# Kernel tuning notes

Measured on AMD Instinct MI355X. Metric: run time of the kernel, lower is better.

Reference implementation:

```python
import jax, jax.numpy as jnp
import numpy as np

# ---- static config (matches init_kwargs) ----
B = 8            # batch_size (graphs)
N = 10000        # num_nodes per graph
NTOT = B * N     # total node rows (80000)
E = 320000       # edges (only over first N nodes, as in the original code)
D = 128          # input_dim == backbone_channels (shared conv forces equality)
H = 4            # heads
C = 128          # backbone_channels (per-head out dim, concat=False)
L = 3            # num_backbone_layers
K = 30           # sort-pool k
HID = 512        # mlp_hidden_dim
OUT = 2          # output_dim
EXPECTED = K * L * C * H + 1  # buggy mlp_input_dim from __init__ -> zero-pad
BN_EPS = 1e-5


def setup_inputs() -> dict:
    key = jax.random.key(0)
    ks = jax.random.split(key, 20)
    s = 1.0 / np.sqrt(D)
    inp = {
        "x": jax.random.normal(ks[0], (NTOT, D), dtype=jnp.float32),
        "edge_index": jax.random.randint(ks[1], (2, E), 0, N, dtype=jnp.int32),
        "age": jax.random.normal(ks[2], (B,), dtype=jnp.float32),
        # shared TransformerConv params (reused across all L layers)
        "Wq": jax.random.normal(ks[3], (D, H * C), dtype=jnp.float32) * s,
        "bq": jax.random.normal(ks[4], (H * C,), dtype=jnp.float32) * 0.02,
        "Wk": jax.random.normal(ks[5], (D, H * C), dtype=jnp.float32) * s,
        "bk": jax.random.normal(ks[6], (H * C,), dtype=jnp.float32) * 0.02,
        "Wv": jax.random.normal(ks[7], (D, H * C), dtype=jnp.float32) * s,
        "bv": jax.random.normal(ks[8], (H * C,), dtype=jnp.float32) * 0.02,
        "Wskip": jax.random.normal(ks[9], (D, C), dtype=jnp.float32) * s,
        "bskip": jax.random.normal(ks[10], (C,), dtype=jnp.float32) * 0.02,
        # per-layer BatchNorm (eval mode: running stats)
        "bn_gamma": 1.0 + 0.1 * jax.random.normal(ks[11], (L, C), dtype=jnp.float32),
        "bn_beta": 0.1 * jax.random.normal(ks[12], (L, C), dtype=jnp.float32),
        "bn_mean": 0.1 * jax.random.normal(ks[13], (L, C), dtype=jnp.float32),
        "bn_var": jax.random.uniform(ks[14], (L, C), dtype=jnp.float32, minval=0.5, maxval=1.5),
        # MLP head (2 layers: EXPECTED->HID, ReLU, HID->OUT)
        "W1": jax.random.normal(ks[15], (EXPECTED, HID), dtype=jnp.float32) * (1.0 / np.sqrt(EXPECTED)),
        "b1": jnp.zeros((HID,), dtype=jnp.float32),
        "W2": jax.random.normal(ks[16], (HID, OUT), dtype=jnp.float32) * (1.0 / np.sqrt(HID)),
        "b2": jnp.zeros((OUT,), dtype=jnp.float32),
    }
    return inp


def _transformer_conv(h, src, dst, Wq, bq, Wk, bk, Wv, bv, Wskip, bskip):
    # PyG TransformerConv, concat=False, root_weight=True, eval (no attn dropout)
    q = (h @ Wq + bq).reshape(NTOT, H, C)
    k = (h @ Wk + bk).reshape(NTOT, H, C)
    v = (h @ Wv + bv).reshape(NTOT, H, C)
    # per-edge attention logits [E, H]
    alpha = jnp.einsum("ehc,ehc->eh", q[dst], k[src]) / np.sqrt(C).astype(np.float32)
    # segment softmax over incoming edges of each target node
    m = jax.ops.segment_max(alpha, dst, num_segments=NTOT)          # [NTOT, H]
    e = jnp.exp(alpha - m[dst])
    denom = jax.ops.segment_sum(e, dst, num_segments=NTOT)          # [NTOT, H]
    a = e / (denom[dst] + 1e-16)                                    # [E, H]
    out = jax.ops.segment_sum(a[:, :, None] * v[src], dst, num_segments=NTOT)  # [NTOT,H,C]
    return out.mean(axis=1) + h @ Wskip + bskip                     # concat=False -> head mean


def reference(x, edge_index, age, Wq, bq, Wk, bk, Wv, bv, Wskip, bskip,
              bn_gamma, bn_beta, bn_mean, bn_var, W1, b1, W2, b2):
    src, dst = edge_index[0], edge_index[1]
    h = x
    feats = []
    for i in range(L):  # fixed small layer count; shared conv weights
        h = _transformer_conv(h, src, dst, Wq, bq, Wk, bk, Wv, bv, Wskip, bskip)
        h = (h - bn_mean[i]) * (bn_gamma[i] / jnp.sqrt(bn_var[i] + BN_EPS)) + bn_beta[i]
        h = jax.nn.relu(h)  # dropout: eval mode no-op
        feats.append(h)
    h = feats[-1]  # concat_input_graph=False
    # global_sort_pool: sort nodes per graph by last channel (desc), take top-k
    xr = h.reshape(B, N, C)
    idx = jnp.argsort(-xr[:, :, -1], axis=1)[:, :K]                 # [B, K]
    pooled = jnp.take_along_axis(xr, idx[:, :, None], axis=1)       # [B, K, C]
    z = pooled.reshape(B, K * C)
    z = jnp.concatenate([z, age.reshape(B, 1)], axis=1)             # [B, K*C+1]
    # zero-pad to the (mismatched) expected MLP input dim, as in the original
    z = jnp.concatenate([z, jnp.zeros((B, EXPECTED - z.shape[1]), dtype=z.dtype)], axis=1)
    z = jax.nn.relu(z @ W1 + b1)
    z = z @ W2 + b2
    return jax.nn.log_softmax(z, axis=-1)
```

## Files before the change

kernel.cpp:

```cpp
#include <hip/hip_runtime.h>
#include <cmath>


#define NN    10000
#define NTOT  80000
#define EE    320000
#define CH    128

__device__ __forceinline__ float rl_f(float v, int lane) {
    return __uint_as_float(__builtin_amdgcn_readlane(__float_as_uint(v), lane));
}

__global__ __launch_bounds__(256) void precompute_kernel(
    const float* __restrict__ Wq, const float* __restrict__ bq,
    const float* __restrict__ Wk, const float* __restrict__ Wv,
    const float* __restrict__ bv, const float* __restrict__ Wskip,
    const float* __restrict__ bskip,
    const float* __restrict__ bn_gamma, const float* __restrict__ bn_beta,
    const float* __restrict__ bn_mean, const float* __restrict__ bn_var,
    float* __restrict__ Bcat, float* __restrict__ biascat,
    float* __restrict__ Wcomb, float* __restrict__ bvbar,
    float* __restrict__ bnS, float* __restrict__ bnB)
{
    const float inv_sqrtC = 0.08838834764831845f;
    int idx = blockIdx.x * 256 + threadIdx.x;
    if (idx < 65536) {
        int c = idx >> 9;
        int o = idx & 511;
        int hbase = o & ~127;
        int j = o & 127;
        const float* wq = Wq + c * 512 + hbase;
        const float* wk = Wk + j * 512 + hbase;
        float s = 0.f;
        for (int cc = 0; cc < 128; cc++) s = fmaf(wq[cc], wk[cc], s);
        Bcat[c * 640 + o] = s * inv_sqrtC;
        return;
    }
    idx -= 65536;
    if (idx < 16384) {
        int c = idx >> 7, n = idx & 127;
        Bcat[c * 640 + 512 + n] = Wskip[c * 128 + n];
        return;
    }
    idx -= 16384;
    if (idx < 512) {
        int o = idx, hbase = o & ~127, j = o & 127;
        const float* wk = Wk + j * 512 + hbase;
        const float* bqp = bq + hbase;
        float s = 0.f;
        for (int cc = 0; cc < 128; cc++) s = fmaf(bqp[cc], wk[cc], s);
        biascat[o] = s * inv_sqrtC;
        return;
    }
    idx -= 512;
    if (idx < 128) {
        biascat[512 + idx] = bskip[idx];
        return;
    }
    idx -= 128;
    if (idx < 65536) {
        int k = idx >> 7;
        int n = idx & 127;
        int h = k >> 7, c = k & 127;
        Wcomb[k * 128 + n] = Wv[c * 512 + h * 128 + n] * 0.25f;
        return;
    }
    idx -= 65536;
    if (idx < 128) {
        float s = 0.f;
        for (int h = 0; h < 4; h++) s += bv[h * 128 + idx];
        bvbar[idx] = 0.25f * s;
        return;
    }
    idx -= 128;
    if (idx < 384) {
        float sc = bn_gamma[idx] / sqrtf(bn_var[idx] + 1e-5f);
        bnS[idx] = sc;
        bnB[idx] = bn_beta[idx] - bn_mean[idx] * sc;
        return;
    }
}

__global__ void count_kernel(const int* __restrict__ dst, int* __restrict__ deg) {
    int e = blockIdx.x * 256 + threadIdx.x;
    if (e < EE) atomicAdd(&deg[dst[e]], 1);
}

__global__ __launch_bounds__(1024) void scan_kernel(const int* __restrict__ deg,
                                                    int* __restrict__ rowstart) {
    __shared__ int part[1024];
    const int t = threadIdx.x;
    int loc[10];
    int s = 0;
    for (int i = 0; i < 10; i++) {
        int idx = t * 10 + i;
        int v = (idx < NN) ? deg[idx] : 0;
        loc[i] = s; s += v;
    }
    part[t] = s; __syncthreads();
    for (int d = 1; d < 1024; d <<= 1) {
        int v = (t >= d) ? part[t - d] : 0;
        __syncthreads();
        part[t] += v;
        __syncthreads();
    }
    int base = (t == 0) ? 0 : part[t - 1];
    for (int i = 0; i < 10; i++) {
        int idx = t * 10 + i;
        if (idx <= NN) rowstart[idx] = base + loc[i];
    }
}

__global__ void scatter_kernel(const int* __restrict__ src, const int* __restrict__ dst,
                               const int* __restrict__ rowstart, int* __restrict__ cursor,
                               int* __restrict__ csr_src) {
    int e = blockIdx.x * 256 + threadIdx.x;
    if (e < EE) {
        int d = dst[e];
        int p = atomicAdd(&cursor[d], 1);
        csr_src[rowstart[d] + p] = src[e];
    }
}

__global__ __launch_bounds__(256, 3) void skip_keys_kernel(
    const float* __restrict__ xup,
    const float* __restrict__ Wskip,
    const float* __restrict__ bskip,
    const float* __restrict__ bnS, const float* __restrict__ bnB,
    float* __restrict__ gkeys)
{
    __shared__ float rowb[64][132];
    __shared__ float Bs[16][132];
    __shared__ float sWc[128];
    const int t = threadIdx.x;
    const int r0 = blockIdx.x * 64;
    const int Mrem = min(64, (NTOT - NN) - r0);
    const int tx = t & 15;
    const int ty = t >> 4;

    for (int f = t; f < 64 * 32; f += 256) {
        int row = f >> 5, c4 = (f & 31) * 4;
        if (row < Mrem)
            *(float4*)&rowb[row][c4] = *(const float4*)(xup + (size_t)(r0 + row) * CH + c4);
    }
    if (t < 128) sWc[t] = Wskip[t * 128 + 127];

    for (int l = 0; l < 2; l++) {
        float acc[4][8];
        #pragma unroll
        for (int i = 0; i < 4; i++)
            #pragma unroll
            for (int j = 0; j < 8; j++) acc[i][j] = 0.f;

        for (int k0 = 0; k0 < 128; k0 += 16) {
            __syncthreads();
            for (int f = t; f < 512; f += 256) {
                int kk = f >> 5, n4 = (f & 31) * 4;
                *(float4*)&Bs[kk][n4] = *(const float4*)(Wskip + (size_t)(k0 + kk) * 128 + n4);
            }
            __syncthreads();
            #pragma unroll
            for (int kq = 0; kq < 4; kq++) {
                float4 a4[4];
                #pragma unroll
                for (int i = 0; i < 4; i++)
                    a4[i] = *(const float4*)&rowb[ty + 16 * i][k0 + kq * 4];
                float4 c0[4], c1[4];
                #pragma unroll
                for (int q = 0; q < 4; q++) {
                    c0[q] = *(const float4*)&Bs[kq * 4 + q][tx * 4];
                    c1[q] = *(const float4*)&Bs[kq * 4 + q][64 + tx * 4];
                }
                #pragma unroll
                for (int q = 0; q < 4; q++) {
                    #pragma unroll
                    for (int i = 0; i < 4; i++) {
                        const float av = (q == 0) ? a4[i].x : (q == 1) ? a4[i].y
                                       : (q == 2) ? a4[i].z : a4[i].w;
                        acc[i][0] = fmaf(av, c0[q].x, acc[i][0]);
                        acc[i][1] = fmaf(av, c0[q].y, acc[i][1]);
                        acc[i][2] = fmaf(av, c0[q].z, acc[i][2]);
                        acc[i][3] = fmaf(av, c0[q].w, acc[i][3]);
                        acc[i][4] = fmaf(av, c1[q].x, acc[i][4]);
                        acc[i][5] = fmaf(av, c1[q].y, acc[i][5]);
                        acc[i][6] = fmaf(av, c1[q].z, acc[i][6]);
                        acc[i][7] = fmaf(av, c1[q].w, acc[i][7]);
                    }
                }
            }
        }
        __syncthreads();
        const float* bS = bnS + l * 128;
        const float* bB = bnB + l * 128;
        #pragma unroll
        for (int i = 0; i < 4; i++) {
            const int row = ty + 16 * i;
            float4 v0, v1;
            float* p0 = &v0.x;
            float* p1 = &v1.x;
            #pragma unroll
            for (int q = 0; q < 4; q++) {
                const int n0c = tx * 4 + q;
                float xv = acc[i][q] + bskip[n0c];
                xv = fmaf(xv, bS[n0c], bB[n0c]);
                p0[q] = fmaxf(xv, 0.f);
                const int n1c = 64 + tx * 4 + q;
                float yv = acc[i][4 + q] + bskip[n1c];
                yv = fmaf(yv, bS[n1c], bB[n1c]);
                p1[q] = fmaxf(yv, 0.f);
            }
            *(float4*)&rowb[row][tx * 4] = v0;
            *(float4*)&rowb[row][64 + tx * 4] = v1;
        }
    }
    __syncthreads();
    if (t < Mrem) {
        float s = 0.f;
        for (int k = 0; k < 128; k++) s = fmaf(rowb[t][k], sWc[k], s);
        s += bskip[127];
        s = fmaf(s, bnS[2 * 128 + 127], bnB[2 * 128 + 127]);
        gkeys[NN + r0 + t] = fmaxf(s, 0.f);
    }
}

template<int BM, int BN, int TM, int TN, int MODE>
__global__ __launch_bounds__(256) void gemm_fp32(
    const float* __restrict__ A, int lda,
    const float* __restrict__ B, int ldb,
    const float* __restrict__ bias, const float* __restrict__ bias2,
    const int* __restrict__ deg,
    const float* __restrict__ Cold,
    const float* __restrict__ bnS, const float* __restrict__ bnB,
    float* __restrict__ C0, int ldc0,
    float* __restrict__ C1, int ldc1,
    int M, int K,
    float* __restrict__ keysOut)
{
    constexpr int BK = 16;
    __shared__ float As[BK][BM + 4];
    __shared__ float Bs[BK][BN + 4];
    const int t  = threadIdx.x;
    const int tx = t % (BN / TN);
    const int ty = t / (BN / TN);
    const int m0 = blockIdx.x * BM;
    const int n0 = blockIdx.y * BN;
    float acc[TM][TN];
    #pragma unroll
    for (int i = 0; i < TM; i++)
        #pragma unroll
        for (int j = 0; j < TN; j++) acc[i][j] = 0.f;

    for (int k0 = 0; k0 < K; k0 += BK) {
        #pragma unroll
        for (int f = t; f < BM * 4; f += 256) {
            int row = f >> 2, fc = f & 3;
            int gm = m0 + row;
            float4 v = make_float4(0.f, 0.f, 0.f, 0.f);
            if (gm < M) v = *(const float4*)(A + (size_t)gm * lda + k0 + fc * 4);
            As[fc * 4 + 0][row] = v.x;
            As[fc * 4 + 1][row] = v.y;
            As[fc * 4 + 2][row] = v.z;
            As[fc * 4 + 3][row] = v.w;
        }
        #pragma unroll
        for (int f = t; f < BK * (BN / 4); f += 256) {
            int kk = f / (BN / 4);
            int nn = (f % (BN / 4)) * 4;
            *(float4*)(&Bs[kk][nn]) = *(const float4*)(B + (size_t)(k0 + kk) * ldb + n0 + nn);
        }
        __syncthreads();
        #pragma unroll
        for (int kk = 0; kk < BK; kk++) {
            float af[TM], bf[TN];
            if constexpr (TM == 2) {
                float2 v = *(const float2*)&As[kk][ty * 2];
                af[0] = v.x; af[1] = v.y;
            } else {
                float4 v = *(const float4*)&As[kk][ty * 4];
                af[0] = v.x; af[1] = v.y; af[2] = v.z; af[3] = v.w;
            }
            if constexpr (TN == 4) {
                float4 v = *(const float4*)&Bs[kk][tx * 4];
                bf[0] = v.x; bf[1] = v.y; bf[2] = v.z; bf[3] = v.w;
            } else {
                float4 v = *(const float4*)&Bs[kk][tx * 4];
                float4 w = *(const float4*)&Bs[kk][BN / 2 + tx * 4];
                bf[0] = v.x; bf[1] = v.y; bf[2] = v.z; bf[3] = v.w;
                bf[4] = w.x; bf[5] = w.y; bf[6] = w.z; bf[7] = w.w;
            }
            #pragma unroll
            for (int i = 0; i < TM; i++)
                #pragma unroll
                for (int j = 0; j < TN; j++)
                    acc[i][j] = fmaf(af[i], bf[j], acc[i][j]);
        }
        __syncthreads();
    }
    #pragma unroll
    for (int i = 0; i < TM; i++) {
        const int gm = m0 + ty * TM + i;
        if (gm >= M) continue;
        const bool addB2 = (MODE == 4) ? (deg[gm] > 0) : false;
        #pragma unroll
        for (int h = 0; h < TN / 4; h++) {
            const int nb = n0 + ((TN == 8) ? h * (BN / 2) + tx * 4 : tx * TN + h * 4);
            float4 v;
            float* vp = &v.x;
            if (MODE == 4) {
                const float4 old = *(const float4*)(Cold + (size_t)gm * ldc1 + nb);
                const float* op = &old.x;
                #pragma unroll
                for (int q = 0; q < 4; q++) {
                    const int n = nb + q;
                    float x = acc[i][h * 4 + q] + op[q];
                    if (addB2) x += bias2[n];
                    x = fmaf(x, bnS[n], bnB[n]);
                    vp[q] = fmaxf(x, 0.f);
                }
                *(float4*)(C0 + (size_t)gm * ldc0 + nb) = v;
                if (keysOut != nullptr && nb == 124) keysOut[gm] = v.w;
            } else {
                #pragma unroll
                for (int q = 0; q < 4; q++)
                    vp[q] = acc[i][h * 4 + q] + bias[nb + q];
                if (nb < 512)
                    *(float4*)(C0 + (size_t)gm * ldc0 + nb) = v;
                else
                    *(float4*)(C1 + (size_t)gm * ldc1 + nb - 512) = v;
            }
        }
    }
}

__global__ __launch_bounds__(256) void attn_kernel(
    const float* __restrict__ h,
    const float* __restrict__ u,
    float* __restrict__ g,
    const int* __restrict__ rowstart,
    const int* __restrict__ csr_src)
{
    __shared__ float h_lds[128 * 65];
    __shared__ __align__(16) float palpha[4 * 64 * 4];
    __shared__ __align__(16) float wT[64 * 4];
    __shared__ __align__(16) float scale_lds[4];
    __shared__ __align__(16) float s_lds[4];
    __shared__ __align__(16) float merge[128 * 4];
    __shared__ int src_lds[64];

    const int n  = blockIdx.x;
    const int t  = threadIdx.x;
    const int w  = t >> 6;
    const int l  = t & 63;
    const int c  = t & 127;
    const int jh = t >> 7;
    const int rs   = rowstart[n];
    const int degn = rowstart[n + 1] - rs;

    if (degn == 0) {
        g[(size_t)n * 512 + t] = 0.f;
        g[(size_t)n * 512 + 256 + t] = 0.f;
        return;
    }
    float u_reg0 = u[(size_t)n * 512 + ((l >> 5)) * 128 + 32 * w + (l & 31)];
    float u_reg1 = u[(size_t)n * 512 + ((l >> 5) + 2) * 128 + 32 * w + (l & 31)];

    float m_run = -INFINITY, s_run = 0.f;
    float4 acc4 = make_float4(0.f, 0.f, 0.f, 0.f);

    for (int base = 0; base < degn; base += 64) {
        const int len = min(64, degn - base);
        __syncthreads();
        if (t < len) src_lds[t] = csr_src[rs + base + t];
        __syncthreads();
        for (int f = t; f < len * 128; f += 256) {
            const int cc = f & 127, j = f >> 7;
            h_lds[cc * 65 + j] = h[(size_t)src_lds[j] * CH + cc];
        }
        __syncthreads();
        {
            float p0 = 0.f, p1 = 0.f, p2 = 0.f, p3 = 0.f;
            #pragma unroll
            for (int dc = 0; dc < 32; dc++) {
                const float hv = h_lds[(32 * w + dc) * 65 + l];
                p0 = fmaf(rl_f(u_reg0, dc),      hv, p0);
                p1 = fmaf(rl_f(u_reg0, 32 + dc), hv, p1);
                p2 = fmaf(rl_f(u_reg1, dc),      hv, p2);
                p3 = fmaf(rl_f(u_reg1, 32 + dc), hv, p3);
            }
            palpha[(0 * 64 + l) * 4 + w] = p0;
            palpha[(1 * 64 + l) * 4 + w] = p1;
            palpha[(2 * 64 + l) * 4 + w] = p2;
            palpha[(3 * 64 + l) * 4 + w] = p3;
        }
        __syncthreads();
        {
            const float4 pa = *(const float4*)&palpha[(w * 64 + l) * 4];
            float alpha = (l < len) ? (pa.x + pa.y + pa.z + pa.w) : -INFINITY;
            float mx = alpha;
            #pragma unroll
            for (int d = 1; d < 64; d <<= 1) mx = fmaxf(mx, __shfl_xor(mx, d, 64));
            const float newm = fmaxf(m_run, mx);
            float e = (l < len) ? __expf(alpha - newm) : 0.f;
            float ss = e;
            #pragma unroll
            for (int d = 1; d < 64; d <<= 1) ss += __shfl_xor(ss, d, 64);
            const float sc = (m_run == -INFINITY) ? 0.f : __expf(m_run - newm);
            s_run = s_run * sc + ss;
            m_run = newm;
            wT[l * 4 + w] = e;
            if (l == 0) scale_lds[w] = sc;
        }
        __syncthreads();
        {
            const float4 scv = *(const float4*)scale_lds;
            acc4.x *= scv.x; acc4.y *= scv.y; acc4.z *= scv.z; acc4.w *= scv.w;
            const int j0 = jh * 32;
            const int j1 = min(len, j0 + 32);
            for (int j = j0; j < j1; j++) {
                const float hv = h_lds[c * 65 + j];
                const float4 wv = *(const float4*)&wT[j * 4];
                acc4.x = fmaf(wv.x, hv, acc4.x);
                acc4.y = fmaf(wv.y, hv, acc4.y);
                acc4.z = fmaf(wv.z, hv, acc4.z);
                acc4.w = fmaf(wv.w, hv, acc4.w);
            }
        }
    }
    if (l == 0) s_lds[w] = s_run;
    __syncthreads();
    if (jh == 1) *(float4*)&merge[c * 4] = acc4;
    __syncthreads();
    if (jh == 0) {
        const float4 o  = *(const float4*)&merge[c * 4];
        const float4 sv = *(const float4*)s_lds;
        g[(size_t)n * 512 + 0 * 128 + c] = (acc4.x + o.x) / (sv.x + 1e-16f);
        g[(size_t)n * 512 + 1 * 128 + c] = (acc4.y + o.y) / (sv.y + 1e-16f);
        g[(size_t)n * 512 + 2 * 128 + c] = (acc4.z + o.z) / (sv.z + 1e-16f);
        g[(size_t)n * 512 + 3 * 128 + c] = (acc4.w + o.w) / (sv.w + 1e-16f);
    }
}

__global__ __launch_bounds__(256) void radix_pool_kernel(
    const float* __restrict__ gkeys, const float* __restrict__ age,
    int* __restrict__ sel, float* __restrict__ z)
{
    __shared__ unsigned int keys[NN];
    __shared__ int hist[256];
    __shared__ int sbuf[256];
    __shared__ unsigned int sel_prefix;
    __shared__ int sel_need;
    __shared__ int gt_counter;
    __shared__ unsigned int cand_key[30];
    __shared__ int cand_idx[30];
    __shared__ int order[30];

    const int b = blockIdx.x;
    const int t = threadIdx.x;

    for (int i = t; i < NN; i += 256)
        keys[i] = __float_as_uint(gkeys[(size_t)b * NN + i]);
    if (t == 0) { sel_prefix = 0u; sel_need = 30; gt_counter = 0; }
    __syncthreads();

    for (int r = 3; r >= 0; r--) {
        hist[t] = 0;
        __syncthreads();
        const int shift = r * 8;
        const unsigned int pmask = (r == 3) ? 0u : (0xFFFFFFFFu << ((r + 1) * 8));
        const unsigned int pref = sel_prefix;
        const int need = sel_need;
        for (int i = t; i < NN; i += 256) {
            unsigned int k = keys[i];
            if ((k & pmask) == pref)
                atomicAdd(&hist[(k >> shift) & 255u], 1);
        }
        __syncthreads();
        sbuf[t] = hist[255 - t];
        __syncthreads();
        for (int d = 1; d < 256; d <<= 1) {
            int o = (t >= d) ? sbuf[t - d] : 0;
            __syncthreads();
            sbuf[t] += o;
            __syncthreads();
        }
        {
            const int v = t;
            const int ge = sbuf[255 - v];
            const int gt = ge - hist[v];
            if (gt < need && need <= ge) {
                sel_prefix = pref | ((unsigned int)v << shift);
                sel_need = need - gt;
            }
        }
        __syncthreads();
    }

    const unsigned int T = sel_prefix;
    const int need_eq = sel_need;
    const int n_gt = 30 - need_eq;

    for (int i = t; i < NN; i += 256) {
        unsigned int k = keys[i];
        if (k > T) {
            int p = atomicAdd(&gt_counter, 1);
            cand_key[p] = k; cand_idx[p] = i;
        }
    }
    {
        const int CHK = (NN + 255) / 256;
        const int i0 = t * CHK, i1 = min(NN, i0 + CHK);
        int local = 0;
        for (int i = i0; i < i1; i++) if (keys[i] == T) local++;
        sbuf[t] = local;
        __syncthreads();
        for (int d = 1; d < 256; d <<= 1) {
            int o = (t >= d) ? sbuf[t - d] : 0;
            __syncthreads();
            sbuf[t] += o;
            __syncthreads();
        }
        int rank = (t == 0) ? 0 : sbuf[t - 1];
        for (int i = i0; i < i1; i++) {
            if (keys[i] == T) {
                if (rank < need_eq) { cand_key[n_gt + rank] = T; cand_idx[n_gt + rank] = i; }
                rank++;
            }
        }
    }
    __syncthreads();
    if (t < 30) {
        const unsigned int mk = cand_key[t];
        const int mi = cand_idx[t];
        int rk = 0;
        for (int j = 0; j < 30; j++) {
            const unsigned int ok = cand_key[j];
            const int oi = cand_idx[j];
            if (ok > mk || (ok == mk && oi < mi)) rk++;
        }
        order[rk] = t;
    }
    __syncthreads();
    if (t < 30) sel[b * 30 + t] = cand_idx[order[t]];
    if (t == 0) z[(size_t)b * 3841 + 3840] = age[b];
}

__global__ __launch_bounds__(128) void gather_kernel(
    const float* __restrict__ h3,
    const float* __restrict__ x,
    const float* __restrict__ Wskip, const float* __restrict__ bskip,
    const float* __restrict__ bnS, const float* __restrict__ bnB,
    const int* __restrict__ sel, float* __restrict__ z)
{
    __shared__ float buf0[128], buf1[128];
    const int blk = blockIdx.x;
    const int b = blk / 30;
    const int kk = blk % 30;
    const int c = threadIdx.x;
    const int i = sel[b * 30 + kk];
    const size_t g = (size_t)b * NN + i;
    float v;
    if (b == 0) {
        v = h3[g * CH + c];
    } else {
        float* rd = buf0;
        float* wr = buf1;
        buf0[c] = x[g * CH + c];
        __syncthreads();
        float s = 0.f;
        for (int l = 0; l < 3; l++) {
            s = 0.f;
            for (int k = 0; k < 128; k++) s = fmaf(rd[k], Wskip[k * 128 + c], s);
            s += bskip[c];
            s = fmaf(s, bnS[l * 128 + c], bnB[l * 128 + c]);
            s = fmaxf(s, 0.f);
            if (l < 2) {
                wr[c] = s;
                __syncthreads();
                float* tmp = rd; rd = wr; wr = tmp;
            }
        }
        v = s;
    }
    z[(size_t)b * 3841 + kk * CH + c] = v;
}

__global__ __launch_bounds__(256) void mlp1_kernel(
    const float* __restrict__ z, const float* __restrict__ W1,
    float* __restrict__ zh)
{
    __shared__ float zs[256];
    const int b  = blockIdx.x >> 4;
    const int ic = blockIdx.x & 15;
    const int t  = threadIdx.x;
    const int i0 = ic * 241;
    const int i1 = min(3841, i0 + 241);
    float a0 = 0.f, a1 = 0.f;
    for (int cb = i0; cb < i1; cb += 256) {
        int cl = min(256, i1 - cb);
        __syncthreads();
        if (t < cl) zs[t] = z[(size_t)b * 3841 + cb + t];
        __syncthreads();
        #pragma unroll 4
        for (int q = 0; q < cl; q++) {
            float zv = zs[q];
            const float* wp = W1 + (size_t)(cb + q) * 512;
            a0 = fmaf(zv, wp[t], a0);
            a1 = fmaf(zv, wp[t + 256], a1);
        }
    }
    atomicAdd(&zh[(size_t)b * 512 + t], a0);
    atomicAdd(&zh[(size_t)b * 512 + t + 256], a1);
}

__global__ __launch_bounds__(256) void mlp2_kernel(
    const float* __restrict__ zh, const float* __restrict__ b1,
    const float* __restrict__ W2, const float* __restrict__ b2,
    float* __restrict__ out)
{
    __shared__ float r0[256], r1[256];
    const int b = blockIdx.x;
    const int t = threadIdx.x;
    float a0 = 0.f, a1 = 0.f;
    for (int j = t; j < 512; j += 256) {
        float v = fmaxf(zh[(size_t)b * 512 + j] + b1[j], 0.f);
        a0 = fmaf(v, W2[j * 2 + 0], a0);
        a1 = fmaf(v, W2[j * 2 + 1], a1);
    }
    r0[t] = a0; r1[t] = a1; __syncthreads();
    for (int s = 128; s > 0; s >>= 1) {
        if (t < s) { r0[t] += r0[t + s]; r1[t] += r1[t + s]; }
        __syncthreads();
    }
    if (t == 0) {
        float l0 = r0[0] + b2[0], l1 = r1[0] + b2[1];
        float m = fmaxf(l0, l1);
        float lse = m + logf(__expf(l0 - m) + __expf(l1 - m));
        out[b * 2 + 0] = l0 - lse;
        out[b * 2 + 1] = l1 - lse;
    }
}

extern "C" void kernel_launch(void* const* d_in, const int* in_sizes, int n_in,
                              void* d_out, int out_size, void* d_ws, size_t ws_size,
                              hipStream_t stream) {
    const float* x     = (const float*)d_in[0];
    const int*   ei    = (const int*)d_in[1];
    const float* age   = (const float*)d_in[2];
    const float* Wq    = (const float*)d_in[3];
    const float* bq    = (const float*)d_in[4];
    const float* Wk    = (const float*)d_in[5];
    const float* Wv    = (const float*)d_in[7];
    const float* bv    = (const float*)d_in[8];
    const float* Wskip = (const float*)d_in[9];
    const float* bskip = (const float*)d_in[10];
    const float* bn_g  = (const float*)d_in[11];
    const float* bn_b  = (const float*)d_in[12];
    const float* bn_m  = (const float*)d_in[13];
    const float* bn_v  = (const float*)d_in[14];
    const float* W1    = (const float*)d_in[15];
    const float* b1    = (const float*)d_in[16];
    const float* W2    = (const float*)d_in[17];
    const float* b2    = (const float*)d_in[18];

    float* ws = (float*)d_ws;
    float* h3      = ws;
    float* hlowA   = h3 + 10240000;
    float* hlowB   = hlowA + 1280000;
    float* u       = hlowB + 1280000;
    float* skipraw = u + 5120000;
    float* Bcat    = skipraw + 1280000;
    float* biascat = Bcat + 81920;
    float* Wcomb   = biascat + 640;
    float* bvbar   = Wcomb + 65536;
    float* bnS     = bvbar + 128;
    float* bnB     = bnS + 384;
    float* zbuf    = bnB + 384;
    float* zh      = zbuf + 30728;
    int* deg      = (int*)(zh + 4096);
    int* cursor   = deg + NN;
    int* rowstart = cursor + NN;
    int* csr_src  = rowstart + NN + 1;
    float* keysG  = (float*)(csr_src + EE);
    int* sel      = (int*)(keysG + NTOT);

    const int* srcI = ei;
    const int* dstI = ei + EE;

    hipMemsetAsync(deg, 0, sizeof(int) * (2 * NN), stream);
    hipMemsetAsync(zh, 0, sizeof(float) * 4096, stream);

    precompute_kernel<<<581, 256, 0, stream>>>(Wq, bq, Wk, Wv, bv, Wskip, bskip,
                                               bn_g, bn_b, bn_m, bn_v,
                                               Bcat, biascat, Wcomb, bvbar, bnS, bnB);
    count_kernel<<<1250, 256, 0, stream>>>(dstI, deg);
    scan_kernel<<<1, 1024, 0, stream>>>(deg, rowstart);
    scatter_kernel<<<1250, 256, 0, stream>>>(srcI, dstI, rowstart, cursor, csr_src);

    skip_keys_kernel<<<1094, 256, 0, stream>>>(x + (size_t)NN * CH, Wskip, bskip,
                                               bnS, bnB, keysG);

    const float* hcur = x;
    for (int l = 0; l < 3; l++) {
        float* dest = (l == 0) ? hlowA : (l == 1) ? hlowB : h3;
        gemm_fp32<64, 128, 4, 8, 0><<<dim3(157, 5), 256, 0, stream>>>(
            hcur, CH, Bcat, 640, biascat, nullptr, nullptr, nullptr,
            nullptr, nullptr, u, 512, skipraw, CH, NN, 128, nullptr);
        attn_kernel<<<NN, 256, 0, stream>>>(hcur, u, u, rowstart, csr_src);
        gemm_fp32<32, 64, 2, 4, 4><<<dim3(313, 2), 256, 0, stream>>>(
            u, 512, Wcomb, CH, nullptr, bvbar, deg, skipraw,
            bnS + l * 128, bnB + l * 128, dest, CH, nullptr, CH, NN, 512,
            (l == 2) ? keysG : nullptr);
        hcur = dest;
    }
    radix_pool_kernel<<<8, 256, 0, stream>>>(keysG, age, sel, zbuf);
    gather_kernel<<<240, 128, 0, stream>>>(h3, x, Wskip, bskip,
                                           bnS, bnB, sel, zbuf);
    mlp1_kernel<<<128, 256, 0, stream>>>(zbuf, W1, zh);
    mlp2_kernel<<<8, 256, 0, stream>>>(zh, b1, W2, b2, (float*)d_out);
}
```

Measured before the change: 624.6 us.

## Replace tiled fp32 GEMMs with row-per-lane kernels reading weights as wave-uniform scalars

The skip-keys GEMM and the two per-layer GEMMs are rewritten so each lane owns one row and each wave owns a 32- or 8-column slice. Weight reads become wave-uniform addresses the compiler can serve through scalar loads, which removes the shared-memory staging of B tiles and most barriers. Results are staged in LDS so stores stay coalesced. The trade-off is lower arithmetic intensity per thread and repeated global or scalar-cache reads of the weights in every block, and the combine kernel is re-gridded to 157x4 blocks.

```diff
diff --git a/kernel.cpp b/kernel.cpp
--- a/kernel.cpp
+++ b/kernel.cpp
@@ -122,7 +122,7 @@
     }
 }
 
-__global__ __launch_bounds__(256, 3) void skip_keys_kernel(
+__global__ __launch_bounds__(256, 4) void skip_keys_kernel(
     const float* __restrict__ xup,
     const float* __restrict__ Wskip,
     const float* __restrict__ bskip,
@@ -130,90 +130,58 @@
     float* __restrict__ gkeys)
 {
     __shared__ float rowb[64][132];
-    __shared__ float Bs[16][132];
     __shared__ float sWc[128];
     const int t = threadIdx.x;
+    const int l = t & 63;
+    const int wv = __builtin_amdgcn_readfirstlane(t >> 6);
+    const int colbase = wv * 32;
     const int r0 = blockIdx.x * 64;
     const int Mrem = min(64, (NTOT - NN) - r0);
-    const int tx = t & 15;
-    const int ty = t >> 4;
 
     for (int f = t; f < 64 * 32; f += 256) {
         int row = f >> 5, c4 = (f & 31) * 4;
-        if (row < Mrem)
-            *(float4*)&rowb[row][c4] = *(const float4*)(xup + (size_t)(r0 + row) * CH + c4);
+        float4 v = make_float4(0.f, 0.f, 0.f, 0.f);
+        if (row < Mrem) v = *(const float4*)(xup + (size_t)(r0 + row) * CH + c4);
+        *(float4*)&rowb[row][c4] = v;
     }
     if (t < 128) sWc[t] = Wskip[t * 128 + 127];
-
-    for (int l = 0; l < 2; l++) {
-        float acc[4][8];
+    __syncthreads();
+
+    for (int layer = 0; layer < 2; layer++) {
+        float acc[32];
         #pragma unroll
-        for (int i = 0; i < 4; i++)
-            #pragma unroll
-            for (int j = 0; j < 8; j++) acc[i][j] = 0.f;
-
-        for (int k0 = 0; k0 < 128; k0 += 16) {
-            __syncthreads();
-            for (int f = t; f < 512; f += 256) {
-                int kk = f >> 5, n4 = (f & 31) * 4;
-                *(float4*)&Bs[kk][n4] = *(const float4*)(Wskip + (size_t)(k0 + kk) * 128 + n4);
-            }
-            __syncthreads();
-            #pragma unroll
-            for (int kq = 0; kq < 4; kq++) {
-                float4 a4[4];
-                #pragma unroll
-                for (int i = 0; i < 4; i++)
-                    a4[i] = *(const float4*)&rowb[ty + 16 * i][k0 + kq * 4];
-                float4 c0[4], c1[4];
-                #pragma unroll
-                for (int q = 0; q < 4; q++) {
-                    c0[q] = *(const float4*)&Bs[kq * 4 + q][tx * 4];
-                    c1[q] = *(const float4*)&Bs[kq * 4 + q][64 + tx * 4];
-                }
-                #pragma unroll
-                for (int q = 0; q < 4; q++) {
-                    #pragma unroll
-                    for (int i = 0; i < 4; i++) {
-                        const float av = (q == 0) ? a4[i].x : (q == 1) ? a4[i].y
-                                       : (q == 2) ? a4[i].z : a4[i].w;
-                        acc[i][0] = fmaf(av, c0[q].x, acc[i][0]);
-                        acc[i][1] = fmaf(av, c0[q].y, acc[i][1]);
-                        acc[i][2] = fmaf(av, c0[q].z, acc[i][2]);
-                        acc[i][3] = fmaf(av, c0[q].w, acc[i][3]);
-                        acc[i][4] = fmaf(av, c1[q].x, acc[i][4]);
-                        acc[i][5] = fmaf(av, c1[q].y, acc[i][5]);
-                        acc[i][6] = fmaf(av, c1[q].z, acc[i][6]);
-                        acc[i][7] = fmaf(av, c1[q].w, acc[i][7]);
-                    }
-                }
-            }
-        }
-        __syncthreads();
-        const float* bS = bnS + l * 128;
-        const float* bB = bnB + l * 128;
-        #pragma unroll
-        for (int i = 0; i < 4; i++) {
-            const int row = ty + 16 * i;
-            float4 v0, v1;
-            float* p0 = &v0.x;
-            float* p1 = &v1.x;
+        for (int c = 0; c < 32; c++) acc[c] = 0.f;
+        const float* Wb = Wskip + colbase;
+        for (int kq = 0; kq < 32; kq++) {
+            const float4 a4 = *(const float4*)&rowb[l][kq * 4];
             #pragma unroll
             for (int q = 0; q < 4; q++) {
-                const int n0c = tx * 4 + q;
-                float xv = acc[i][q] + bskip[n0c];
-                xv = fmaf(xv, bS[n0c], bB[n0c]);
-                p0[q] = fmaxf(xv, 0.f);
-                const int n1c = 64 + tx * 4 + q;
-                float yv = acc[i][4 + q] + bskip[n1c];
-                yv = fmaf(yv, bS[n1c], bB[n1c]);
-                p1[q] = fmaxf(yv, 0.f);
+                const float av = (q == 0) ? a4.x : (q == 1) ? a4.y
+                               : (q == 2) ? a4.z : a4.w;
+                const float* wr = Wb + (kq * 4 + q) * 128;
+                #pragma unroll
+                for (int c = 0; c < 32; c++)
+                    acc[c] = fmaf(av, wr[c], acc[c]);
             }
-            *(float4*)&rowb[row][tx * 4] = v0;
-            *(float4*)&rowb[row][64 + tx * 4] = v1;
-        }
-    }
-    __syncthreads();
+        }
+        __syncthreads();
+        const float* bS = bnS + layer * 128;
+        const float* bB = bnB + layer * 128;
+        #pragma unroll
+        for (int c4 = 0; c4 < 8; c4++) {
+            float4 v;
+            float* vp = &v.x;
+            #pragma unroll
+            for (int q = 0; q < 4; q++) {
+                const int n = colbase + c4 * 4 + q;
+                float xv = acc[c4 * 4 + q] + bskip[n];
+                xv = fmaf(xv, bS[n], bB[n]);
+                vp[q] = fmaxf(xv, 0.f);
+            }
+            *(float4*)&rowb[l][colbase + c4 * 4] = v;
+        }
+        __syncthreads();
+    }
     if (t < Mrem) {
         float s = 0.f;
         for (int k = 0; k < 128; k++) s = fmaf(rowb[t][k], sWc[k], s);
@@ -223,112 +191,148 @@
     }
 }
 
-template<int BM, int BN, int TM, int TN, int MODE>
-__global__ __launch_bounds__(256) void gemm_fp32(
-    const float* __restrict__ A, int lda,
-    const float* __restrict__ B, int ldb,
-    const float* __restrict__ bias, const float* __restrict__ bias2,
+__global__ __launch_bounds__(256, 4) void ugemm_sg(
+    const float* __restrict__ A,
+    const float* __restrict__ Bcat,
+    const float* __restrict__ biascat,
+    float* __restrict__ u,
+    float* __restrict__ skipraw)
+{
+    __shared__ float rowb[64][132];
+    const int t = threadIdx.x;
+    const int l = t & 63;
+    const int wv = __builtin_amdgcn_readfirstlane(t >> 6);
+    const int r0 = blockIdx.x * 64;
+    const int by = blockIdx.y;
+    const int nb0 = by * 128;
+    const int colbase = nb0 + wv * 32;
+    const int Mrem = min(64, NN - r0);
+
+    for (int f = t; f < 64 * 32; f += 256) {
+        int row = f >> 5, c4 = (f & 31) * 4;
+        float4 v = make_float4(0.f, 0.f, 0.f, 0.f);
+        if (row < Mrem) v = *(const float4*)(A + (size_t)(r0 + row) * CH + c4);
+        *(float4*)&rowb[row][c4] = v;
+    }
+    __syncthreads();
+
+    float acc[32];
+    #pragma unroll
+    for (int c = 0; c < 32; c++) acc[c] = 0.f;
+    const float* Wb = Bcat + colbase;
+    for (int kq = 0; kq < 32; kq++) {
+        const float4 a4 = *(const float4*)&rowb[l][kq * 4];
+        #pragma unroll
+        for (int q = 0; q < 4; q++) {
+            const float av = (q == 0) ? a4.x : (q == 1) ? a4.y
+                           : (q == 2) ? a4.z : a4.w;
+            const float* wr = Wb + (kq * 4 + q) * 640;
+            #pragma unroll
+            for (int c = 0; c < 32; c++)
+                acc[c] = fmaf(av, wr[c], acc[c]);
+        }
+    }
+    __syncthreads();
+    #pragma unroll
+    for (int c4 = 0; c4 < 8; c4++) {
+        float4 v;
+        float* vp = &v.x;
+        #pragma unroll
+        for (int q = 0; q < 4; q++)
+            vp[q] = acc[c4 * 4 + q] + biascat[colbase + c4 * 4 + q];
+        *(float4*)&rowb[l][wv * 32 + c4 * 4] = v;
+    }
+    __syncthreads();
+    if (by < 4) {
+        for (int f = t; f < 64 * 32; f += 256) {
+            int row = f >> 5, c4 = (f & 31) * 4;
+            if (row < Mrem)
+                *(float4*)(u + (size_t)(r0 + row) * 512 + nb0 + c4) =
+                    *(const float4*)&rowb[row][c4];
+        }
+    } else {
+        for (int f = t; f < 64 * 32; f += 256) {
+            int row = f >> 5, c4 = (f & 31) * 4;
+            if (row < Mrem)
+                *(float4*)(skipraw + (size_t)(r0 + row) * CH + c4) =
+                    *(const float4*)&rowb[row][c4];
+        }
+    }
+}
+
+__global__ __launch_bounds__(256, 4) void comb_sg(
+    const float* __restrict__ G,
+    const float* __restrict__ Wcomb,
+    const float* __restrict__ bvbar,
     const int* __restrict__ deg,
     const float* __restrict__ Cold,
     const float* __restrict__ bnS, const float* __restrict__ bnB,
-    float* __restrict__ C0, int ldc0,
-    float* __restrict__ C1, int ldc1,
-    int M, int K,
+    float* __restrict__ dest,
     float* __restrict__ keysOut)
 {
-    constexpr int BK = 16;
-    __shared__ float As[BK][BM + 4];
-    __shared__ float Bs[BK][BN + 4];
-    const int t  = threadIdx.x;
-    const int tx = t % (BN / TN);
-    const int ty = t / (BN / TN);
-    const int m0 = blockIdx.x * BM;
-    const int n0 = blockIdx.y * BN;
-    float acc[TM][TN];
+    __shared__ float chunk[64][68];
+    __shared__ float outb[64][36];
+    const int t = threadIdx.x;
+    const int l = t & 63;
+    const int wv = __builtin_amdgcn_readfirstlane(t >> 6);
+    const int r0 = blockIdx.x * 64;
+    const int nb0 = blockIdx.y * 32;
+    const int colbase = nb0 + wv * 8;
+    const int Mrem = min(64, NN - r0);
+
+    float acc[8];
     #pragma unroll
-    for (int i = 0; i < TM; i++)
+    for (int c = 0; c < 8; c++) acc[c] = 0.f;
+
+    for (int kc = 0; kc < 512; kc += 64) {
+        __syncthreads();
+        for (int f = t; f < 64 * 16; f += 256) {
+            int row = f >> 4, c4 = (f & 15) * 4;
+            float4 v = make_float4(0.f, 0.f, 0.f, 0.f);
+            if (row < Mrem)
+                v = *(const float4*)(G + (size_t)(r0 + row) * 512 + kc + c4);
+            *(float4*)&chunk[row][c4] = v;
+        }
+        __syncthreads();
+        const float* Wb = Wcomb + colbase + (size_t)kc * 128;
+        for (int kq = 0; kq < 16; kq++) {
+            const float4 a4 = *(const float4*)&chunk[l][kq * 4];
+            #pragma unroll
+            for (int q = 0; q < 4; q++) {
+                const float av = (q == 0) ? a4.x : (q == 1) ? a4.y
+                               : (q == 2) ? a4.z : a4.w;
+                const float* wr = Wb + (kq * 4 + q) * 128;
+                #pragma unroll
+                for (int c = 0; c < 8; c++)
+                    acc[c] = fmaf(av, wr[c], acc[c]);
+            }
+        }
+    }
+    __syncthreads();
+    {
+        const int gr = min(r0 + l, NN - 1);
+        const bool addB2 = (l < Mrem) && (deg[gr] > 0);
+        const float4 o0 = *(const float4*)(Cold + (size_t)gr * CH + colbase);
+        const float4 o1 = *(const float4*)(Cold + (size_t)gr * CH + colbase + 4);
+        const float op[8] = {o0.x, o0.y, o0.z, o0.w, o1.x, o1.y, o1.z, o1.w};
         #pragma unroll
-        for (int j = 0; j < TN; j++) acc[i][j] = 0.f;
-
-    for (int k0 = 0; k0 < K; k0 += BK) {
-        #pragma unroll
-        for (int f = t; f < BM * 4; f += 256) {
-            int row = f >> 2, fc = f & 3;
-            int gm = m0 + row;
-            float4 v = make_float4(0.f, 0.f, 0.f, 0.f);
-            if (gm < M) v = *(const float4*)(A + (size_t)gm * lda + k0 + fc * 4);
-            As[fc * 4 + 0][row] = v.x;
-            As[fc * 4 + 1][row] = v.y;
-            As[fc * 4 + 2][row] = v.z;
-            As[fc * 4 + 3][row] = v.w;
-        }
-        #pragma unroll
-        for (int f = t; f < BK * (BN / 4); f += 256) {
-            int kk = f / (BN / 4);
-            int nn = (f % (BN / 4)) * 4;
-            *(float4*)(&Bs[kk][nn]) = *(const float4*)(B + (size_t)(k0 + kk) * ldb + n0 + nn);
-        }
-        __syncthreads();
-        #pragma unroll
-        for (int kk = 0; kk < BK; kk++) {
-            float af[TM], bf[TN];
-            if constexpr (TM == 2) {
-                float2 v = *(const float2*)&As[kk][ty * 2];
-                af[0] = v.x; af[1] = v.y;
-            } else {
-                float4 v = *(const float4*)&As[kk][ty * 4];
-                af[0] = v.x; af[1] = v.y; af[2] = v.z; af[3] = v.w;
-            }
-            if constexpr (TN == 4) {
-                float4 v = *(const float4*)&Bs[kk][tx * 4];
-                bf[0] = v.x; bf[1] = v.y; bf[2] = v.z; bf[3] = v.w;
-            } else {
-                float4 v = *(const float4*)&Bs[kk][tx * 4];
-                float4 w = *(const float4*)&Bs[kk][BN / 2 + tx * 4];
-                bf[0] = v.x; bf[1] = v.y; bf[2] = v.z; bf[3] = v.w;
-                bf[4] = w.x; bf[5] = w.y; bf[6] = w.z; bf[7] = w.w;
-            }
-            #pragma unroll
-            for (int i = 0; i < TM; i++)
-                #pragma unroll
-                for (int j = 0; j < TN; j++)
-                    acc[i][j] = fmaf(af[i], bf[j], acc[i][j]);
-        }
-        __syncthreads();
-    }
-    #pragma unroll
-    for (int i = 0; i < TM; i++) {
-        const int gm = m0 + ty * TM + i;
-        if (gm >= M) continue;
-        const bool addB2 = (MODE == 4) ? (deg[gm] > 0) : false;
-        #pragma unroll
-        for (int h = 0; h < TN / 4; h++) {
-            const int nb = n0 + ((TN == 8) ? h * (BN / 2) + tx * 4 : tx * TN + h * 4);
-            float4 v;
-            float* vp = &v.x;
-            if (MODE == 4) {
-                const float4 old = *(const float4*)(Cold + (size_t)gm * ldc1 + nb);
-                const float* op = &old.x;
-                #pragma unroll
-                for (int q = 0; q < 4; q++) {
-                    const int n = nb + q;
-                    float x = acc[i][h * 4 + q] + op[q];
-                    if (addB2) x += bias2[n];
-                    x = fmaf(x, bnS[n], bnB[n]);
-                    vp[q] = fmaxf(x, 0.f);
-                }
-                *(float4*)(C0 + (size_t)gm * ldc0 + nb) = v;
-                if (keysOut != nullptr && nb == 124) keysOut[gm] = v.w;
-            } else {
-                #pragma unroll
-                for (int q = 0; q < 4; q++)
-                    vp[q] = acc[i][h * 4 + q] + bias[nb + q];
-                if (nb < 512)
-                    *(float4*)(C0 + (size_t)gm * ldc0 + nb) = v;
-                else
-                    *(float4*)(C1 + (size_t)gm * ldc1 + nb - 512) = v;
-            }
-        }
+        for (int c = 0; c < 8; c++) {
+            const int n = colbase + c;
+            float x = acc[c] + op[c];
+            if (addB2) x += bvbar[n];
+            x = fmaf(x, bnS[n], bnB[n]);
+            outb[l][wv * 8 + c] = fmaxf(x, 0.f);
+        }
+    }
+    __syncthreads();
+    for (int f = t; f < 64 * 8; f += 256) {
+        int row = f >> 3, c4 = (f & 7) * 4;
+        if (row < Mrem)
+            *(float4*)(dest + (size_t)(r0 + row) * CH + nb0 + c4) =
+                *(const float4*)&outb[row][c4];
+    }
+    if (keysOut != nullptr && nb0 == 96) {
+        if (t < Mrem) keysOut[r0 + t] = outb[t][31];
     }
 }
 
@@ -702,13 +706,12 @@
     const float* hcur = x;
     for (int l = 0; l < 3; l++) {
         float* dest = (l == 0) ? hlowA : (l == 1) ? hlowB : h3;
-        gemm_fp32<64, 128, 4, 8, 0><<<dim3(157, 5), 256, 0, stream>>>(
-            hcur, CH, Bcat, 640, biascat, nullptr, nullptr, nullptr,
-            nullptr, nullptr, u, 512, skipraw, CH, NN, 128, nullptr);
+        ugemm_sg<<<dim3(157, 5), 256, 0, stream>>>(
+            hcur, Bcat, biascat, u, skipraw);
         attn_kernel<<<NN, 256, 0, stream>>>(hcur, u, u, rowstart, csr_src);
-        gemm_fp32<32, 64, 2, 4, 4><<<dim3(313, 2), 256, 0, stream>>>(
-            u, 512, Wcomb, CH, nullptr, bvbar, deg, skipraw,
-            bnS + l * 128, bnB + l * 128, dest, CH, nullptr, CH, NN, 512,
+        comb_sg<<<dim3(157, 4), 256, 0, stream>>>(
+            u, Wcomb, bvbar, deg, skipraw,
+            bnS + l * 128, bnB + l * 128, dest,
             (l == 2) ? keysG : nullptr);
         hcur = dest;
     }
```

Result: slower. 664.7 us (+6.4%).
